# Kernel optimization log

Measured on AMD Instinct MI355X. Metric: run time of the kernel, lower is better.

The kernel has to match this reference:

```python
import jax, jax.numpy as jnp
import numpy as np

WS = 7          # window size
SHIFT = WS // 2 # shift for odd blocks
NH = 8          # num heads
EPS = 1e-5


def _rel_pos_index(ws):
    coords = np.stack(np.meshgrid(np.arange(ws), np.arange(ws), indexing='ij'))  # (2, ws, ws)
    cf = coords.reshape(2, -1)                                  # (2, N)
    rc = (cf[:, :, None] - cf[:, None, :]).transpose(1, 2, 0)   # (N, N, 2)
    rc[..., 0] += ws - 1
    rc[..., 1] += ws - 1
    rc[..., 0] *= 2 * ws - 1
    return rc.sum(-1)  # (N, N) int


def _attn_mask(Hp, Wp, ws, shift):
    # (nW, N, N) additive mask with 0 / -100, as in the torch code
    img = np.zeros((Hp, Wp), dtype=np.float32)
    cnt = 0
    slices = (slice(0, -ws), slice(-ws, -shift), slice(-shift, None))
    for h in slices:
        for w in slices:
            img[h, w] = cnt
            cnt += 1
    mw = img.reshape(Hp // ws, ws, Wp // ws, ws).transpose(0, 2, 1, 3).reshape(-1, ws * ws)
    am = mw[:, None, :] - mw[:, :, None]
    return np.where(am != 0, -100.0, 0.0).astype(np.float32)


def _layernorm(x, w, b):
    m = x.mean(-1, keepdims=True)
    v = ((x - m) ** 2).mean(-1, keepdims=True)
    return (x - m) * jax.lax.rsqrt(v + EPS) * w + b


def _window_partition(x, ws):
    B, H, W, C = x.shape
    x = x.reshape(B, H // ws, ws, W // ws, ws, C).transpose(0, 1, 3, 2, 4, 5)
    return x.reshape(-1, ws * ws, C)


def _window_reverse(w, ws, H, W):
    B = w.shape[0] // (H // ws * W // ws)
    x = w.reshape(B, H // ws, W // ws, ws, ws, -1).transpose(0, 1, 3, 2, 4, 5)
    return x.reshape(B, H, W, -1)


def _window_msa(xw, qkv_w, qkv_b, proj_w, proj_b, rpb, rel_idx, mask):
    Bw, N, C = xw.shape
    hd = C // NH
    qkv = (xw @ qkv_w.T + qkv_b).reshape(Bw, N, 3, NH, hd).transpose(2, 0, 3, 1, 4)
    q, k, v = qkv[0] * (hd ** -0.5), qkv[1], qkv[2]
    attn = jnp.einsum('bhnd,bhmd->bhnm', q, k)                      # (Bw, NH, N, N)
    bias = rpb[rel_idx.reshape(-1)].reshape(N, N, NH).transpose(2, 0, 1)
    attn = attn + bias[None]
    if mask is not None:
        nW = mask.shape[0]
        attn = attn.reshape(Bw // nW, nW, NH, N, N) + mask[None, :, None]
        attn = attn.reshape(Bw, NH, N, N)
    attn = jax.nn.softmax(attn, axis=-1)
    out = jnp.einsum('bhnm,bhmd->bhnd', attn, v).transpose(0, 2, 1, 3).reshape(Bw, N, C)
    return out @ proj_w.T + proj_b


def _forward(x, ln1_w, ln1_b, qkv_w, qkv_b, proj_w, proj_b, rpb,
             ln2_w, ln2_b, mlp_w1, mlp_b1, mlp_w2, mlp_b2, H, W):
    B, L, C = x.shape
    rel_idx = _rel_pos_index(WS)
    pad_r = (WS - W % WS) % WS
    pad_b = (WS - H % WS) % WS
    Hp, Wp = H + pad_b, W + pad_r
    depth = ln1_w.shape[0]
    for i in range(depth):
        shift = 0 if i % 2 == 0 else SHIFT
        shortcut = x
        h = _layernorm(x, ln1_w[i], ln1_b[i]).reshape(B, H, W, C)
        if pad_r > 0 or pad_b > 0:
            h = jnp.pad(h, ((0, 0), (0, pad_b), (0, pad_r), (0, 0)))
        if shift > 0:
            h = jnp.roll(h, (-shift, -shift), axis=(1, 2))
            mask = jnp.asarray(_attn_mask(Hp, Wp, WS, shift))
        else:
            mask = None
        hw = _window_partition(h, WS)
        hw = _window_msa(hw, qkv_w[i], qkv_b[i], proj_w[i], proj_b[i], rpb[i], rel_idx, mask)
        h = _window_reverse(hw.reshape(-1, WS, WS, C), WS, Hp, Wp)
        if shift > 0:
            h = jnp.roll(h, (shift, shift), axis=(1, 2))
        if pad_r > 0 or pad_b > 0:
            h = h[:, :H, :W, :]
        x = shortcut + h.reshape(B, H * W, C)
        m = _layernorm(x, ln2_w[i], ln2_b[i])
        m = jax.nn.gelu(m @ mlp_w1[i].T + mlp_b1[i], approximate=False)
        x = x + (m @ mlp_w2[i].T + mlp_b2[i])
    return x


def setup_inputs() -> dict:
    key = jax.random.key(0)
    ks = jax.random.split(key, 8)
    B, H, W, C, D = 8, 112, 112, 256, 2
    hid = 4 * C
    return {
        'x': jax.random.normal(ks[0], (B, H * W, C), jnp.float32),
        'ln1_w': jnp.ones((D, C), jnp.float32),
        'ln1_b': jnp.zeros((D, C), jnp.float32),
        'qkv_w': jax.random.normal(ks[1], (D, 3 * C, C), jnp.float32) * 0.02,
        'qkv_b': jnp.zeros((D, 3 * C), jnp.float32),
        'proj_w': jax.random.normal(ks[2], (D, C, C), jnp.float32) * 0.02,
        'proj_b': jnp.zeros((D, C), jnp.float32),
        'rpb': jax.random.normal(ks[3], (D, (2 * WS - 1) ** 2, NH), jnp.float32) * 0.02,
        'ln2_w': jnp.ones((D, C), jnp.float32),
        'ln2_b': jnp.zeros((D, C), jnp.float32),
        'mlp_w1': jax.random.normal(ks[4], (D, hid, C), jnp.float32) * 0.02,
        'mlp_b1': jnp.zeros((D, hid), jnp.float32),
        'mlp_w2': jax.random.normal(ks[5], (D, C, hid), jnp.float32) * 0.02,
        'mlp_b2': jnp.zeros((D, C), jnp.float32),
        'H': H,
        'W': W,
    }


def reference(x, ln1_w, ln1_b, qkv_w, qkv_b, proj_w, proj_b, rpb,
              ln2_w, ln2_b, mlp_w1, mlp_b1, mlp_w2, mlp_b2, H, W):
    return _forward(x, ln1_w, ln1_b, qkv_w, qkv_b, proj_w, proj_b, rpb,
                    ln2_w, ln2_b, mlp_w1, mlp_b1, mlp_w2, mlp_b2, H, W)
```

## Files before the change

### kernel.cpp

```cpp
#include <hip/hip_runtime.h>

typedef unsigned short u16;
typedef unsigned int u32;
typedef __attribute__((ext_vector_type(8))) short bf16x8;
typedef __attribute__((ext_vector_type(4))) float f32x4;
typedef __attribute__((ext_vector_type(16))) float f32x16;
typedef __attribute__((ext_vector_type(8))) unsigned short u16x8;
typedef const __attribute__((address_space(1))) void gvoid;
typedef __attribute__((address_space(3))) void svoid;

#define T_TOK 100352
#define CDIM 256
#define ATTN_SCALE 0.17677669529663687f

__device__ __forceinline__ u16 f2bf(float f) {
    u32 u = __float_as_uint(f);
    u32 r = (u + 0x7fffu + ((u >> 16) & 1u)) >> 16;
    return (u16)r;
}
__device__ __forceinline__ float bf2f(u16 h) {
    return __uint_as_float(((u32)h) << 16);
}
__device__ __forceinline__ float gelu_f(float x) {
    return 0.5f * x * (1.0f + erff(x * 0.70710678118654752f));
}
__device__ __forceinline__ int div7(int q) { return (q * 37) >> 8; }
__device__ __forceinline__ int reg3(int r) { return r < 105 ? 0 : (r < 109 ? 1 : 2); }

__global__ void cvt_kernel(const float* __restrict__ in, u16* __restrict__ out, int n) {
    int i = blockIdx.x * 256 + threadIdx.x;
    if (i < n) out[i] = f2bf(in[i]);
}

__global__ __launch_bounds__(256) void ln_kernel(
    const float* __restrict__ X, const float* __restrict__ w,
    const float* __restrict__ b, u16* __restrict__ Y)
{
    int wid = threadIdx.x >> 6, l = threadIdx.x & 63;
    int t = blockIdx.x * 4 + wid;
    const float4 x4 = ((const float4*)(X + (size_t)t * CDIM))[l];
    float s  = x4.x + x4.y + x4.z + x4.w;
    float s2 = x4.x*x4.x + x4.y*x4.y + x4.z*x4.z + x4.w*x4.w;
    #pragma unroll
    for (int o = 32; o; o >>= 1) { s += __shfl_xor(s, o); s2 += __shfl_xor(s2, o); }
    float mean = s * (1.0f/256.0f);
    float var  = s2 * (1.0f/256.0f) - mean*mean;
    float rstd = rsqrtf(var + 1e-5f);
    float4 w4 = ((const float4*)w)[l];
    float4 b4 = ((const float4*)b)[l];
    ushort4 o4;
    o4.x = f2bf((x4.x - mean)*rstd*w4.x + b4.x);
    o4.y = f2bf((x4.y - mean)*rstd*w4.y + b4.y);
    o4.z = f2bf((x4.z - mean)*rstd*w4.z + b4.z);
    o4.w = f2bf((x4.w - mean)*rstd*w4.w + b4.w);
    ((ushort4*)(Y + (size_t)t * CDIM))[l] = o4;
}

template<int EPI>
__global__ __launch_bounds__(256) void gemm_kernel(
    const u16* __restrict__ A, const u16* __restrict__ Bw,
    const float* __restrict__ bias, void* __restrict__ outp,
    const float* __restrict__ res, int N, int K)
{
    __shared__ u16 lsA[128 * 32];
    __shared__ u16 lsB[128 * 32];
    const int l = threadIdx.x & 63;
    const int w = threadIdx.x >> 6;
    const int mT = blockIdx.y, nT = blockIdx.x;
    const int wr = w >> 1, wc = w & 1;

    f32x4 acc[4][4];
    #pragma unroll
    for (int m = 0; m < 4; ++m)
        #pragma unroll
        for (int n = 0; n < 4; ++n) acc[m][n] = (f32x4){0.f,0.f,0.f,0.f};

    const int rsub = l >> 2;
    const int ksub = (l & 3) * 8;

    for (int kt = 0; kt < K; kt += 32) {
        __syncthreads();
        #pragma unroll
        for (int i = 0; i < 2; ++i) {
            int row = i*64 + w*16 + rsub;
            const u16* ga = A  + (size_t)(mT*128 + row) * K + kt + ksub;
            const u16* gb = Bw + (size_t)(nT*128 + row) * K + kt + ksub;
            u16* la = lsA + i*2048 + w*512;
            u16* lb = lsB + i*2048 + w*512;
            __builtin_amdgcn_global_load_lds((gvoid*)ga, (svoid*)la, 16, 0, 0);
            __builtin_amdgcn_global_load_lds((gvoid*)gb, (svoid*)lb, 16, 0, 0);
        }
        __syncthreads();
        const int lr = l & 15;
        const int lk = (l >> 4) * 8;
        bf16x8 a[4], b[4];
        #pragma unroll
        for (int m = 0; m < 4; ++m) a[m] = *(const bf16x8*)&lsA[(wr*64 + m*16 + lr)*32 + lk];
        #pragma unroll
        for (int n = 0; n < 4; ++n) b[n] = *(const bf16x8*)&lsB[(wc*64 + n*16 + lr)*32 + lk];
        #pragma unroll
        for (int m = 0; m < 4; ++m)
            #pragma unroll
            for (int n = 0; n < 4; ++n)
                acc[m][n] = __builtin_amdgcn_mfma_f32_16x16x32_bf16(a[m], b[n], acc[m][n], 0, 0, 0);
    }

    const int lr4 = (l >> 4) * 4;
    const int lcn = l & 15;
    #pragma unroll
    for (int m = 0; m < 4; ++m) {
        #pragma unroll
        for (int n = 0; n < 4; ++n) {
            int row0 = mT*128 + wr*64 + m*16 + lr4;
            int col  = nT*128 + wc*64 + n*16 + lcn;
            float bb = bias[col];
            #pragma unroll
            for (int j = 0; j < 4; ++j) {
                size_t idx = (size_t)(row0 + j) * N + col;
                float v = acc[m][n][j] + bb;
                if (EPI == 0)      ((u16*)outp)[idx] = f2bf(v);
                else if (EPI == 1) ((u16*)outp)[idx] = f2bf(gelu_f(v));
                else               ((float*)outp)[idx] = v + res[idx];
            }
        }
    }
}

__global__ __launch_bounds__(256) void attn_kernel(
    const u16* __restrict__ qkv, const float* __restrict__ rpb,
    u16* __restrict__ outb, int shift)
{
    __shared__ u16 Vt[8][2048];
    __shared__ float biasl[8 * 176];
    __shared__ int tok[64];

    const int t = threadIdx.x;
    const int w = t >> 6;
    const int l = t & 63;
    const int lo = l & 31;
    const int hi = l >> 5;
    const int win = blockIdx.x;
    const int wj = win & 15, wi = (win >> 4) & 15, bb = win >> 8;

    if (t < 64) {
        int qq = t > 48 ? 48 : t;
        int i = div7(qq), j = qq - i*7;
        int rr = wi*7 + i + shift; if (rr >= 112) rr -= 112;
        int cc = wj*7 + j + shift; if (cc >= 112) cc -= 112;
        tok[t] = bb*12544 + rr*112 + cc;
    }
    for (int i2 = t; i2 < 1352; i2 += 256)
        biasl[(i2 & 7)*176 + (i2 >> 3)] = rpb[i2];
    __syncthreads();

    int iqv[2], jqv[2], regq[2];
    #pragma unroll
    for (int nt = 0; nt < 2; ++nt) {
        int q = nt*32 + lo; int qb = q > 48 ? 48 : q;
        int iq = div7(qb), jq = qb - iq*7;
        iqv[nt] = iq; jqv[nt] = jq;
        regq[nt] = 0;
        if (shift > 0) regq[nt] = reg3(wi*7 + iq)*3 + reg3(wj*7 + jq);
    }

    #pragma unroll 1
    for (int hh = 0; hh < 2; ++hh) {
        const int h = 2*w + hh;

        {
            u16x8 vreg[4];
            if (l < 49) {
                const u16x8* vs = (const u16x8*)(qkv + (size_t)tok[l]*768 + 512 + h*32);
                #pragma unroll
                for (int c4 = 0; c4 < 4; ++c4) vreg[c4] = vs[c4];
            } else {
                #pragma unroll
                for (int c4 = 0; c4 < 4; ++c4) vreg[c4] = (u16x8){0,0,0,0,0,0,0,0};
            }
            u16* vt = &Vt[h][0];
            #pragma unroll
            for (int c4 = 0; c4 < 4; ++c4)
                #pragma unroll
                for (int e = 0; e < 8; ++e)
                    vt[(c4*8 + e)*64 + (l ^ (e << 3))] = vreg[c4][e];
        }

        bf16x8 kf[2][2], qf[2][2];
        #pragma unroll
        for (int mt = 0; mt < 2; ++mt)
            #pragma unroll
            for (int td = 0; td < 2; ++td)
                kf[mt][td] = *(const bf16x8*)(qkv + (size_t)tok[mt*32 + lo]*768 + 256 + h*32 + td*16 + hi*8);
        #pragma unroll
        for (int nt = 0; nt < 2; ++nt)
            #pragma unroll
            for (int td = 0; td < 2; ++td)
                qf[nt][td] = *(const bf16x8*)(qkv + (size_t)tok[nt*32 + lo]*768 + h*32 + td*16 + hi*8);

        f32x16 s[2][2];
        #pragma unroll
        for (int mt = 0; mt < 2; ++mt)
            #pragma unroll
            for (int nt = 0; nt < 2; ++nt) {
                f32x16 z;
                #pragma unroll
                for (int i = 0; i < 16; ++i) z[i] = 0.f;
                s[mt][nt] = z;
            }
        #pragma unroll
        for (int td = 0; td < 2; ++td)
            #pragma unroll
            for (int mt = 0; mt < 2; ++mt)
                #pragma unroll
                for (int nt = 0; nt < 2; ++nt)
                    s[mt][nt] = __builtin_amdgcn_mfma_f32_32x32x16_bf16(kf[mt][td], qf[nt][td], s[mt][nt], 0, 0, 0);

        asm volatile("s_waitcnt lgkmcnt(0)" ::: "memory");
        __builtin_amdgcn_sched_barrier(0);

        const float* bh = biasl + h*176;
        #pragma unroll
        for (int mt = 0; mt < 2; ++mt) {
            #pragma unroll
            for (int i = 0; i < 16; ++i) {
                int r = (i & 3) + 8*(i >> 2) + 4*hi;
                int k = mt*32 + r;
                bool valid = k < 49;
                int kb = valid ? k : 48;
                int ik = div7(kb), jk = kb - ik*7;
                int regk = 0;
                if (shift > 0) regk = reg3(wi*7 + ik)*3 + reg3(wj*7 + jk);
                #pragma unroll
                for (int nt = 0; nt < 2; ++nt) {
                    float v = s[mt][nt][i] * ATTN_SCALE
                            + bh[(iqv[nt] - ik + 6)*13 + (jqv[nt] - jk + 6)];
                    if (shift > 0 && regq[nt] != regk) v -= 100.0f;
                    if (!valid) v = -1e30f;
                    s[mt][nt][i] = v;
                }
            }
        }

        #pragma unroll
        for (int nt = 0; nt < 2; ++nt) {
            float mx = -1e30f;
            #pragma unroll
            for (int i = 0; i < 16; ++i) mx = fmaxf(mx, fmaxf(s[0][nt][i], s[1][nt][i]));
            mx = fmaxf(mx, __shfl_xor(mx, 32));
            float sum = 0.f;
            #pragma unroll
            for (int mt = 0; mt < 2; ++mt)
                #pragma unroll
                for (int i = 0; i < 16; ++i) {
                    float e = __expf(s[mt][nt][i] - mx);
                    s[mt][nt][i] = e;
                    sum += e;
                }
            sum += __shfl_xor(sum, 32);
            float inv = __builtin_amdgcn_rcpf(sum);

            u32 pk[2][8];
            #pragma unroll
            for (int mt = 0; mt < 2; ++mt)
                #pragma unroll
                for (int j = 0; j < 8; ++j)
                    pk[mt][j] = (u32)f2bf(s[mt][nt][2*j] * inv)
                              | ((u32)f2bf(s[mt][nt][2*j + 1] * inv) << 16);

            f32x16 o;
            #pragma unroll
            for (int i = 0; i < 16; ++i) o[i] = 0.f;
            #pragma unroll
            for (int kt = 0; kt < 4; ++kt) {
                const int mt = kt >> 1;
                const int base = (kt & 1) * 4;
                u32 a0 = pk[mt][base + 0], a1 = pk[mt][base + 1];
                u32 a2 = pk[mt][base + 2], a3 = pk[mt][base + 3];
                asm volatile("v_permlane32_swap_b32 %0, %1" : "+v"(a0), "+v"(a2));
                asm volatile("v_permlane32_swap_b32 %0, %1" : "+v"(a1), "+v"(a3));
                union { u32 u[4]; bf16x8 v; } pf;
                pf.u[0] = a0; pf.u[1] = a1; pf.u[2] = a2; pf.u[3] = a3;
                bf16x8 vb = *(const bf16x8*)(&Vt[h][lo*64 + ((kt*16 + hi*8) ^ ((lo & 7) << 3))]);
                o = __builtin_amdgcn_mfma_f32_32x32x16_bf16(pf.v, vb, o, 0, 0, 0);
            }

            #pragma unroll
            for (int i = 0; i < 16; ++i) {
                int q = nt*32 + (i & 3) + 8*(i >> 2) + 4*hi;
                if (q < 49)
                    outb[(size_t)tok[q]*256 + h*32 + lo] = f2bf(o[i]);
            }
        }
    }
}

extern "C" void kernel_launch(void* const* d_in, const int* in_sizes, int n_in,
                              void* d_out, int out_size, void* d_ws, size_t ws_size,
                              hipStream_t stream) {
    const float* x_in   = (const float*)d_in[0];
    const float* ln1_w  = (const float*)d_in[1];
    const float* ln1_b  = (const float*)d_in[2];
    const float* qkv_w  = (const float*)d_in[3];
    const float* qkv_b  = (const float*)d_in[4];
    const float* proj_w = (const float*)d_in[5];
    const float* proj_b = (const float*)d_in[6];
    const float* rpb    = (const float*)d_in[7];
    const float* ln2_w  = (const float*)d_in[8];
    const float* ln2_b  = (const float*)d_in[9];
    const float* mlp_w1 = (const float*)d_in[10];
    const float* mlp_b1 = (const float*)d_in[11];
    const float* mlp_w2 = (const float*)d_in[12];
    const float* mlp_b2 = (const float*)d_in[13];
    float* xout = (float*)d_out;

    char* p = (char*)d_ws;
    u16* wq = (u16*)p;  p += (size_t)2*768*256*2;
    u16* wp = (u16*)p;  p += (size_t)2*256*256*2;
    u16* w1 = (u16*)p;  p += (size_t)2*1024*256*2;
    u16* w2 = (u16*)p;  p += (size_t)2*256*1024*2;
    u16* buf_y   = (u16*)p; p += (size_t)T_TOK*256*2;
    u16* buf_big = (u16*)p;

    {
        int n;
        n = 2*768*256;  cvt_kernel<<<(n+255)/256, 256, 0, stream>>>(qkv_w,  wq, n);
        n = 2*256*256;  cvt_kernel<<<(n+255)/256, 256, 0, stream>>>(proj_w, wp, n);
        n = 2*1024*256; cvt_kernel<<<(n+255)/256, 256, 0, stream>>>(mlp_w1, w1, n);
        n = 2*256*1024; cvt_kernel<<<(n+255)/256, 256, 0, stream>>>(mlp_w2, w2, n);
    }

    for (int i = 0; i < 2; ++i) {
        const int shift = (i == 0) ? 0 : 3;
        const float* xcur = (i == 0) ? x_in : xout;

        ln_kernel<<<T_TOK/4, 256, 0, stream>>>(xcur, ln1_w + i*256, ln1_b + i*256, buf_y);
        gemm_kernel<0><<<dim3(6, T_TOK/128), 256, 0, stream>>>(
            buf_y, wq + (size_t)i*768*256, qkv_b + i*768, buf_big, nullptr, 768, 256);
        attn_kernel<<<2048, 256, 0, stream>>>(buf_big, rpb + i*169*8, buf_y, shift);
        gemm_kernel<2><<<dim3(2, T_TOK/128), 256, 0, stream>>>(
            buf_y, wp + (size_t)i*256*256, proj_b + i*256, xout, xcur, 256, 256);
        ln_kernel<<<T_TOK/4, 256, 0, stream>>>(xout, ln2_w + i*256, ln2_b + i*256, buf_y);
        gemm_kernel<1><<<dim3(8, T_TOK/128), 256, 0, stream>>>(
            buf_y, w1 + (size_t)i*1024*256, mlp_b1 + i*1024, buf_big, nullptr, 1024, 256);
        gemm_kernel<2><<<dim3(2, T_TOK/128), 256, 0, stream>>>(
            buf_big, w2 + (size_t)i*256*1024, mlp_b2 + i*256, xout, xout, 256, 1024);
    }
}
```

Baseline: 1.085 ms.

## Double-buffer GEMM LDS with K=64 tiles, XOR swizzle, and XCD-aware block remap

Rewrites the bf16 GEMM main loop to use two LDS buffers with K-step 64. The next tile is loaded via global_load_lds while MFMAs run on the current one, and an XOR swizzle on LDS layout avoids bank conflicts. It also switches to a 1D grid remapped so consecutive tiles land on the same XCD for L2 reuse, and raises wave priority around the MFMA block. The cost is double the LDS footprint (64KB per block), which lowers occupancy.

```diff
diff --git a/kernel.cpp b/kernel.cpp
--- a/kernel.cpp
+++ b/kernel.cpp
@@ -60,14 +60,19 @@
 __global__ __launch_bounds__(256) void gemm_kernel(
     const u16* __restrict__ A, const u16* __restrict__ Bw,
     const float* __restrict__ bias, void* __restrict__ outp,
-    const float* __restrict__ res, int N, int K)
+    const float* __restrict__ res, int N, int K, int nTn)
 {
-    __shared__ u16 lsA[128 * 32];
-    __shared__ u16 lsB[128 * 32];
-    const int l = threadIdx.x & 63;
-    const int w = threadIdx.x >> 6;
-    const int mT = blockIdx.y, nT = blockIdx.x;
+    __shared__ __align__(16) u16 lds[2][2][128 * 64];
+    const int tid = threadIdx.x;
+    const int l = tid & 63;
+    const int w = tid >> 6;
     const int wr = w >> 1, wc = w & 1;
+
+    const int nBlocks = gridDim.x;
+    const int cpx = nBlocks >> 3;
+    const int lin = (blockIdx.x & 7) * cpx + (blockIdx.x >> 3);
+    const int nT = lin % nTn;
+    const int mT = lin / nTn;
 
     f32x4 acc[4][4];
     #pragma unroll
@@ -75,38 +80,71 @@
         #pragma unroll
         for (int n = 0; n < 4; ++n) acc[m][n] = (f32x4){0.f,0.f,0.f,0.f};
 
-    const int rsub = l >> 2;
-    const int ksub = (l & 3) * 8;
-
-    for (int kt = 0; kt < K; kt += 32) {
-        __syncthreads();
-        #pragma unroll
-        for (int i = 0; i < 2; ++i) {
-            int row = i*64 + w*16 + rsub;
-            const u16* ga = A  + (size_t)(mT*128 + row) * K + kt + ksub;
-            const u16* gb = Bw + (size_t)(nT*128 + row) * K + kt + ksub;
-            u16* la = lsA + i*2048 + w*512;
-            u16* lb = lsB + i*2048 + w*512;
-            __builtin_amdgcn_global_load_lds((gvoid*)ga, (svoid*)la, 16, 0, 0);
-            __builtin_amdgcn_global_load_lds((gvoid*)gb, (svoid*)lb, 16, 0, 0);
-        }
-        __syncthreads();
-        const int lr = l & 15;
-        const int lk = (l >> 4) * 8;
-        bf16x8 a[4], b[4];
-        #pragma unroll
-        for (int m = 0; m < 4; ++m) a[m] = *(const bf16x8*)&lsA[(wr*64 + m*16 + lr)*32 + lk];
-        #pragma unroll
-        for (int n = 0; n < 4; ++n) b[n] = *(const bf16x8*)&lsB[(wc*64 + n*16 + lr)*32 + lk];
-        #pragma unroll
-        for (int m = 0; m < 4; ++m)
-            #pragma unroll
-            for (int n = 0; n < 4; ++n)
-                acc[m][n] = __builtin_amdgcn_mfma_f32_16x16x32_bf16(a[m], b[n], acc[m][n], 0, 0, 0);
-    }
-
-    const int lr4 = (l >> 4) * 4;
-    const int lcn = l & 15;
+    const int sr = tid >> 3;
+    const int sg = tid & 7;
+
+    #define STAGE(buf, kt)                                                              \
+        {                                                                               \
+            _Pragma("unroll")                                                           \
+            for (int c = 0; c < 4; ++c) {                                               \
+                int r = c*32 + sr;                                                      \
+                int gsrc = sg ^ (r & 7);                                                \
+                const u16* ga = A  + (size_t)(mT*128 + r) * K + (kt) + gsrc*8;          \
+                const u16* gb = Bw + (size_t)(nT*128 + r) * K + (kt) + gsrc*8;          \
+                u16* la = &lds[buf][0][(c*256 + w*64) * 8];                              \
+                u16* lb = &lds[buf][1][(c*256 + w*64) * 8];                              \
+                __builtin_amdgcn_global_load_lds((gvoid*)ga, (svoid*)la, 16, 0, 0);     \
+                __builtin_amdgcn_global_load_lds((gvoid*)gb, (svoid*)lb, 16, 0, 0);     \
+            }                                                                           \
+        }
+
+    const int nSteps = K >> 6;
+    int cur = 0;
+
+    STAGE(0, 0);
+    asm volatile("s_waitcnt vmcnt(0)" ::: "memory");
+    __builtin_amdgcn_s_barrier();
+    asm volatile("" ::: "memory");
+
+    const int lr = l & 15, gq = l >> 4;
+    for (int t = 0; t < nSteps; ++t) {
+        bf16x8 a[2][4], b[2][4];
+        #pragma unroll
+        for (int kk = 0; kk < 2; ++kk) {
+            #pragma unroll
+            for (int m = 0; m < 4; ++m) {
+                int r = wr*64 + m*16 + lr;
+                int g = kk*4 + gq;
+                a[kk][m] = *(const bf16x8*)&lds[cur][0][r*64 + (g ^ (r & 7))*8];
+            }
+            #pragma unroll
+            for (int n = 0; n < 4; ++n) {
+                int r = wc*64 + n*16 + lr;
+                int g = kk*4 + gq;
+                b[kk][n] = *(const bf16x8*)&lds[cur][1][r*64 + (g ^ (r & 7))*8];
+            }
+        }
+        if (t + 1 < nSteps) STAGE(cur ^ 1, (t + 1) * 64);
+
+        __builtin_amdgcn_s_setprio(1);
+        #pragma unroll
+        for (int kk = 0; kk < 2; ++kk)
+            #pragma unroll
+            for (int m = 0; m < 4; ++m)
+                #pragma unroll
+                for (int n = 0; n < 4; ++n)
+                    acc[m][n] = __builtin_amdgcn_mfma_f32_16x16x32_bf16(a[kk][m], b[kk][n], acc[m][n], 0, 0, 0);
+        __builtin_amdgcn_s_setprio(0);
+
+        asm volatile("s_waitcnt vmcnt(0)" ::: "memory");
+        __builtin_amdgcn_s_barrier();
+        asm volatile("" ::: "memory");
+        cur ^= 1;
+    }
+    #undef STAGE
+
+    const int lr4 = gq * 4;
+    const int lcn = lr;
     #pragma unroll
     for (int m = 0; m < 4; ++m) {
         #pragma unroll
@@ -334,15 +372,15 @@
         const float* xcur = (i == 0) ? x_in : xout;
 
         ln_kernel<<<T_TOK/4, 256, 0, stream>>>(xcur, ln1_w + i*256, ln1_b + i*256, buf_y);
-        gemm_kernel<0><<<dim3(6, T_TOK/128), 256, 0, stream>>>(
-            buf_y, wq + (size_t)i*768*256, qkv_b + i*768, buf_big, nullptr, 768, 256);
+        gemm_kernel<0><<<784*6, 256, 0, stream>>>(
+            buf_y, wq + (size_t)i*768*256, qkv_b + i*768, buf_big, nullptr, 768, 256, 6);
         attn_kernel<<<2048, 256, 0, stream>>>(buf_big, rpb + i*169*8, buf_y, shift);
-        gemm_kernel<2><<<dim3(2, T_TOK/128), 256, 0, stream>>>(
-            buf_y, wp + (size_t)i*256*256, proj_b + i*256, xout, xcur, 256, 256);
+        gemm_kernel<2><<<784*2, 256, 0, stream>>>(
+            buf_y, wp + (size_t)i*256*256, proj_b + i*256, xout, xcur, 256, 256, 2);
         ln_kernel<<<T_TOK/4, 256, 0, stream>>>(xout, ln2_w + i*256, ln2_b + i*256, buf_y);
-        gemm_kernel<1><<<dim3(8, T_TOK/128), 256, 0, stream>>>(
-            buf_y, w1 + (size_t)i*1024*256, mlp_b1 + i*1024, buf_big, nullptr, 1024, 256);
-        gemm_kernel<2><<<dim3(2, T_TOK/128), 256, 0, stream>>>(
-            buf_big, w2 + (size_t)i*256*1024, mlp_b2 + i*256, xout, xout, 256, 1024);
-    }
-}
+        gemm_kernel<1><<<784*8, 256, 0, stream>>>(
+            buf_y, w1 + (size_t)i*1024*256, mlp_b1 + i*1024, buf_big, nullptr, 1024, 256, 8);
+        gemm_kernel<2><<<784*2, 256, 0, stream>>>(
+            buf_big, w2 + (size_t)i*256*1024, mlp_b2 + i*256, xout, xout, 256, 1024, 2);
+    }
+}
```

Result: faster. 1.052 ms (-3.1%).
